# Kernel tuning notes

Measured on AMD Instinct MI355X. Metric: run time of the kernel, lower is better.

## Reference

```python
import jax, jax.numpy as jnp
import numpy as np

N_NODES = 50000
N_EDGES = 800000
D = 128
BN_EPS = 1e-5


def setup_inputs() -> dict:
    key = jax.random.key(0)
    ks = jax.random.split(key, 8)
    scale = 1.0 / np.sqrt(D)
    return {
        "nfeat": jax.random.normal(ks[0], (N_NODES, D), dtype=jnp.float32),
        "efeat": jax.random.normal(ks[1], (N_EDGES, D), dtype=jnp.float32),
        "src": jax.random.randint(ks[2], (N_EDGES,), 0, N_NODES, dtype=jnp.int32),
        "dst": jax.random.randint(ks[3], (N_EDGES,), 0, N_NODES, dtype=jnp.int32),
        "W1": jax.random.normal(ks[4], (D, D), dtype=jnp.float32) * scale,
        "b1": jnp.zeros((D,), dtype=jnp.float32),
        "gamma": jnp.ones((D,), dtype=jnp.float32),
        "beta": jnp.zeros((D,), dtype=jnp.float32),
        "W2": jax.random.normal(ks[5], (D, D), dtype=jnp.float32) * scale,
        "b2": jnp.zeros((D,), dtype=jnp.float32),
        "We": jax.random.normal(ks[6], (D, D), dtype=jnp.float32) * scale,
        "be": jnp.zeros((D,), dtype=jnp.float32),
    }


def reference(nfeat, efeat, src, dst, W1, b1, gamma, beta, W2, b2, We, be):
    n = nfeat.shape[0]
    # GINConv, sum aggregator, eps=0: h = (1+eps)*x + sum_{j in N(i)} x_j
    agg = jax.ops.segment_sum(nfeat[src], dst, num_segments=n)  # [N, D]
    h = nfeat + agg
    # apply_func: Linear -> BatchNorm1d (training-mode batch stats) -> ReLU -> Linear
    h = h @ W1 + b1
    mu = jnp.mean(h, axis=0)
    var = jnp.mean(jnp.square(h - mu), axis=0)  # biased variance, as BatchNorm uses
    h = gamma * (h - mu) * jax.lax.rsqrt(var + BN_EPS) + beta
    h = jax.nn.relu(h)
    h = h @ W2 + b2
    # edge branch: linear on edge feats, scatter-sum to destination nodes, residual add
    e = efeat @ We + be                                          # [E, D]
    h_e = jax.ops.segment_sum(e, dst, num_segments=n)            # [N, D]
    return h + h_e
```

## Files before the change

### kernel.cpp

```cpp
#include <hip/hip_runtime.h>

#define D 128

typedef __attribute__((ext_vector_type(8))) short bf16x8;
typedef __attribute__((ext_vector_type(4))) float f32x4;
typedef __attribute__((ext_vector_type(4))) float fx4;
typedef __attribute__((ext_vector_type(4))) short sx4;

static __device__ __forceinline__ short f2bf(float f) {
    union { float f; unsigned u; } v; v.f = f;
    const unsigned r = v.u + 0x7FFFu + ((v.u >> 16) & 1u);
    return (short)(r >> 16);
}
static __device__ __forceinline__ float bf2f(short s) {
    union { unsigned u; float f; } v;
    v.u = ((unsigned)(unsigned short)s) << 16;
    return v.f;
}

__global__ __launch_bounds__(256) void k_prep(
    const float* __restrict__ nfeat, short* __restrict__ nfb,
    const float* __restrict__ W1, const float* __restrict__ W2,
    const float* __restrict__ We, short* __restrict__ Wt1,
    short* __restrict__ Wt2, short* __restrict__ Wte,
    int* __restrict__ cnt, float* __restrict__ stats,
    int N, int nbConv, int nbW)
{
    const int b = blockIdx.x, t = threadIdx.x;
    if (b < nbConv) {
        const int i = b * 256 + t;
        if (i < (N * D) / 4) {
            const float4 v = ((const float4*)nfeat)[i];
            short4 s;
            s.x = f2bf(v.x); s.y = f2bf(v.y); s.z = f2bf(v.z); s.w = f2bf(v.w);
            ((short4*)nfb)[i] = s;
        }
    } else if (b < nbConv + nbW) {
        const int i = (b - nbConv) * 256 + t;
        const int m = i >> 14;
        const int idx = i & 16383;
        const int k = idx >> 7, n = idx & 127;
        const float* W = (m == 0) ? W1 : (m == 1) ? W2 : We;
        short* Wt = (m == 0) ? Wt1 : (m == 1) ? Wt2 : Wte;
        Wt[n * 128 + k] = f2bf(W[k * 128 + n]);
    } else {
        const int i = (b - nbConv - nbW) * 256 + t;
        if (i * 4 < N) ((int4*)cnt)[i] = make_int4(0, 0, 0, 0);
        if (b == nbConv + nbW && t < 256) stats[t] = 0.f;
    }
}

__global__ void k_hist(const int* __restrict__ dst, int* __restrict__ cnt, int E) {
    const int base = (blockIdx.x * 256 + threadIdx.x) * 4;
    if (base + 3 < E) {
        const int4 d4 = *(const int4*)(dst + base);
        atomicAdd(&cnt[d4.x], 1);
        atomicAdd(&cnt[d4.y], 1);
        atomicAdd(&cnt[d4.z], 1);
        atomicAdd(&cnt[d4.w], 1);
    } else {
        for (int e = base; e < E; ++e) atomicAdd(&cnt[dst[e]], 1);
    }
}

__global__ __launch_bounds__(1024) void k_scan(
    const int* __restrict__ cnt, int* __restrict__ row_ptr,
    int* __restrict__ cursor, float* __restrict__ degf, int N)
{
    __shared__ int ws[17];
    const int t = threadIdx.x, lane = t & 63, wid = t >> 6;
    int carry = 0;
    const int ntiles = (N + 4095) / 4096;
    for (int tile = 0; tile < ntiles; ++tile) {
        const int base = tile * 4096 + t * 4;
        int4 v = make_int4(0, 0, 0, 0);
        if (base + 3 < N) v = *(const int4*)(cnt + base);
        else {
            if (base     < N) v.x = cnt[base];
            if (base + 1 < N) v.y = cnt[base + 1];
            if (base + 2 < N) v.z = cnt[base + 2];
            if (base + 3 < N) v.w = cnt[base + 3];
        }
        const int s = v.x + v.y + v.z + v.w;
        int incl = s;
        #pragma unroll
        for (int off = 1; off < 64; off <<= 1) {
            const int u = __shfl_up(incl, off);
            if (lane >= off) incl += u;
        }
        if (lane == 63) ws[wid] = incl;
        __syncthreads();
        if (t < 16) {
            const int wv = ws[t];
            int wincl = wv;
            #pragma unroll
            for (int off = 1; off < 16; off <<= 1) {
                const int u = __shfl_up(wincl, off);
                if (t >= off) wincl += u;
            }
            ws[t] = wincl - wv;
            if (t == 15) ws[16] = wincl;
        }
        __syncthreads();
        const int ex = carry + ws[wid] + (incl - s);
        if (base + 3 < N) {
            const int4 rp = make_int4(ex, ex + v.x, ex + v.x + v.y,
                                      ex + v.x + v.y + v.z);
            *(int4*)(row_ptr + base) = rp;
            *(int4*)(cursor + base)  = rp;
            *(float4*)(degf + base)  =
                make_float4((float)v.x, (float)v.y, (float)v.z, (float)v.w);
        } else {
            int run = ex;
            if (base < N)     { row_ptr[base]   = run; cursor[base]   = run; degf[base]   = (float)v.x; run += v.x; }
            if (base + 1 < N) { row_ptr[base+1] = run; cursor[base+1] = run; degf[base+1] = (float)v.y; run += v.y; }
            if (base + 2 < N) { row_ptr[base+2] = run; cursor[base+2] = run; degf[base+2] = (float)v.z; run += v.z; }
            if (base + 3 < N) { row_ptr[base+3] = run; cursor[base+3] = run; degf[base+3] = (float)v.w; }
        }
        carry += ws[16];
        __syncthreads();
    }
    if (t == 0) row_ptr[N] = carry;
}

__global__ void k_scatter(const int* __restrict__ src, const int* __restrict__ dst,
                          int* __restrict__ cursor,
                          int2* __restrict__ epair, int E) {
    const int base = (blockIdx.x * 256 + threadIdx.x) * 4;
    if (base + 3 < E) {
        const int4 d4 = *(const int4*)(dst + base);
        const int4 s4 = *(const int4*)(src + base);
        int p;
        p = atomicAdd(&cursor[d4.x], 1); epair[p] = make_int2(base + 0, s4.x);
        p = atomicAdd(&cursor[d4.y], 1); epair[p] = make_int2(base + 1, s4.y);
        p = atomicAdd(&cursor[d4.z], 1); epair[p] = make_int2(base + 2, s4.z);
        p = atomicAdd(&cursor[d4.w], 1); epair[p] = make_int2(base + 3, s4.w);
    } else {
        for (int e = base; e < E; ++e) {
            const int p = atomicAdd(&cursor[dst[e]], 1);
            epair[p] = make_int2(e, src[e]);
        }
    }
}

__global__ __launch_bounds__(256) void k_gather(
    const short* __restrict__ nfb, const float* __restrict__ efeat,
    const int* __restrict__ row_ptr, const int2* __restrict__ epair,
    short* __restrict__ xbuf, short* __restrict__ agg_e, int N)
{
    const int t = threadIdx.x;
    const int c = t & 31;
    const int node = blockIdx.x * 8 + (t >> 5);
    if (node >= N) return;

    const int start = row_ptr[node];
    const int end   = row_ptr[node + 1];

    fx4 an = {0.f, 0.f, 0.f, 0.f};
    fx4 ae = {0.f, 0.f, 0.f, 0.f};
    int e = start;
    for (; e + 3 < end; e += 4) {
        const int2 p0 = epair[e];
        const int2 p1 = epair[e + 1];
        const int2 p2 = epair[e + 2];
        const int2 p3 = epair[e + 3];
        const fx4 ev0 = __builtin_nontemporal_load((const fx4*)(efeat + (size_t)p0.x * D) + c);
        const fx4 ev1 = __builtin_nontemporal_load((const fx4*)(efeat + (size_t)p1.x * D) + c);
        const fx4 ev2 = __builtin_nontemporal_load((const fx4*)(efeat + (size_t)p2.x * D) + c);
        const fx4 ev3 = __builtin_nontemporal_load((const fx4*)(efeat + (size_t)p3.x * D) + c);
        const sx4 nv0 = *((const sx4*)(nfb + (size_t)p0.y * D) + c);
        const sx4 nv1 = *((const sx4*)(nfb + (size_t)p1.y * D) + c);
        const sx4 nv2 = *((const sx4*)(nfb + (size_t)p2.y * D) + c);
        const sx4 nv3 = *((const sx4*)(nfb + (size_t)p3.y * D) + c);
        #pragma unroll
        for (int j = 0; j < 4; ++j) {
            ae[j] += (ev0[j] + ev1[j]) + (ev2[j] + ev3[j]);
            an[j] += (bf2f(nv0[j]) + bf2f(nv1[j])) + (bf2f(nv2[j]) + bf2f(nv3[j]));
        }
    }
    for (; e < end; ++e) {
        const int2 p0 = epair[e];
        const fx4 ev0 = __builtin_nontemporal_load((const fx4*)(efeat + (size_t)p0.x * D) + c);
        const sx4 nv0 = *((const sx4*)(nfb + (size_t)p0.y * D) + c);
        #pragma unroll
        for (int j = 0; j < 4; ++j) {
            ae[j] += ev0[j];
            an[j] += bf2f(nv0[j]);
        }
    }

    const sx4 self = *((const sx4*)(nfb + (size_t)node * D) + c);
    sx4 xv, ev2;
    #pragma unroll
    for (int j = 0; j < 4; ++j) {
        xv[j]  = f2bf(bf2f(self[j]) + an[j]);
        ev2[j] = f2bf(ae[j]);
    }
    __builtin_nontemporal_store(xv,  (sx4*)(xbuf  + (size_t)node * D) + c);
    __builtin_nontemporal_store(ev2, (sx4*)(agg_e + (size_t)node * D) + c);
}

__global__ __launch_bounds__(256) void k_h1(const short* xbuf,
                                            const short* __restrict__ Wt1,
                                            const float* __restrict__ b1,
                                            short* h1,
                                            float* __restrict__ stats, int N) {
    const int t = threadIdx.x;
    const int lane = t & 63;
    const int w = t >> 6;
    const int l15 = lane & 15;
    const int kg = lane >> 4;
    const int row0 = blockIdx.x * 64;

    bf16x8 bfr[4][2];
    #pragma unroll
    for (int kt = 0; kt < 4; ++kt)
        #pragma unroll
        for (int cf = 0; cf < 2; ++cf)
            bfr[kt][cf] = *(const bf16x8*)(Wt1 + (w * 32 + cf * 16 + l15) * D +
                                           kt * 32 + kg * 8);

    f32x4 acc[4][2];
    #pragma unroll
    for (int rt = 0; rt < 4; ++rt) { acc[rt][0] = (f32x4)0.f; acc[rt][1] = (f32x4)0.f; }

    #pragma unroll
    for (int rt = 0; rt < 4; ++rt) {
        const int row = row0 + rt * 16 + l15;
        bf16x8 a0 = (bf16x8)(short)0, a1 = a0, a2 = a0, a3 = a0;
        if (row < N) {
            const short* xp = xbuf + (size_t)row * D + kg * 8;
            a0 = *(const bf16x8*)(xp);
            a1 = *(const bf16x8*)(xp + 32);
            a2 = *(const bf16x8*)(xp + 64);
            a3 = *(const bf16x8*)(xp + 96);
        }
        acc[rt][0] = __builtin_amdgcn_mfma_f32_16x16x32_bf16(a0, bfr[0][0], acc[rt][0], 0, 0, 0);
        acc[rt][1] = __builtin_amdgcn_mfma_f32_16x16x32_bf16(a0, bfr[0][1], acc[rt][1], 0, 0, 0);
        acc[rt][0] = __builtin_amdgcn_mfma_f32_16x16x32_bf16(a1, bfr[1][0], acc[rt][0], 0, 0, 0);
        acc[rt][1] = __builtin_amdgcn_mfma_f32_16x16x32_bf16(a1, bfr[1][1], acc[rt][1], 0, 0, 0);
        acc[rt][0] = __builtin_amdgcn_mfma_f32_16x16x32_bf16(a2, bfr[2][0], acc[rt][0], 0, 0, 0);
        acc[rt][1] = __builtin_amdgcn_mfma_f32_16x16x32_bf16(a2, bfr[2][1], acc[rt][1], 0, 0, 0);
        acc[rt][0] = __builtin_amdgcn_mfma_f32_16x16x32_bf16(a3, bfr[3][0], acc[rt][0], 0, 0, 0);
        acc[rt][1] = __builtin_amdgcn_mfma_f32_16x16x32_bf16(a3, bfr[3][1], acc[rt][1], 0, 0, 0);
    }

    const float bias0 = b1[w * 32 + l15];
    const float bias1 = b1[w * 32 + 16 + l15];
    float cs0 = 0.f, cq0 = 0.f, cs1 = 0.f, cq1 = 0.f;
    #pragma unroll
    for (int rt = 0; rt < 4; ++rt) {
        #pragma unroll
        for (int j = 0; j < 4; ++j) {
            const int row = row0 + rt * 16 + kg * 4 + j;
            if (row < N) {
                const float h0 = acc[rt][0][j] + bias0;
                const float hv = acc[rt][1][j] + bias1;
                h1[(size_t)row * D + w * 32 + l15]      = f2bf(h0);
                h1[(size_t)row * D + w * 32 + 16 + l15] = f2bf(hv);
                cs0 += h0; cq0 += h0 * h0;
                cs1 += hv; cq1 += hv * hv;
            }
        }
    }
    #pragma unroll
    for (int m = 16; m < 64; m <<= 1) {
        cs0 += __shfl_xor(cs0, m); cq0 += __shfl_xor(cq0, m);
        cs1 += __shfl_xor(cs1, m); cq1 += __shfl_xor(cq1, m);
    }
    if (lane < 16) {
        atomicAdd(stats + w * 32 + lane,            cs0);
        atomicAdd(stats + w * 32 + 16 + lane,       cs1);
        atomicAdd(stats + 128 + w * 32 + lane,      cq0);
        atomicAdd(stats + 128 + w * 32 + 16 + lane, cq1);
    }
}

__global__ __launch_bounds__(256) void k_out(const short* __restrict__ h1,
                                             const short* __restrict__ agg_e,
                                             const short* __restrict__ Wt2,
                                             const short* __restrict__ Wte,
                                             const float* __restrict__ stats,
                                             const float* __restrict__ gamma,
                                             const float* __restrict__ beta,
                                             const float* __restrict__ b2,
                                             const float* __restrict__ be,
                                             const float* __restrict__ degf,
                                             float* __restrict__ out, int N) {
    __shared__ float scs[128], shs[128];
    const int t = threadIdx.x;
    if (t < 128) {
        const float invN = 1.0f / (float)N;
        const float mu = stats[t] * invN;
        const float var = stats[128 + t] * invN - mu * mu;
        const float sc = gamma[t] * rsqrtf(var + 1e-5f);
        scs[t] = sc;
        shs[t] = beta[t] - mu * sc;
    }
    __syncthreads();

    const int lane = t & 63;
    const int w = t >> 6;
    const int l15 = lane & 15;
    const int kg = lane >> 4;
    const int row0 = blockIdx.x * 64;

    f32x4 acc[4][2];
    #pragma unroll
    for (int rt = 0; rt < 4; ++rt) { acc[rt][0] = (f32x4)0.f; acc[rt][1] = (f32x4)0.f; }

    bf16x8 bfr[4][2];

    #pragma unroll
    for (int kt = 0; kt < 4; ++kt)
        #pragma unroll
        for (int cf = 0; cf < 2; ++cf)
            bfr[kt][cf] = *(const bf16x8*)(Wt2 + (w * 32 + cf * 16 + l15) * D +
                                           kt * 32 + kg * 8);

    #pragma unroll
    for (int rt = 0; rt < 4; ++rt) {
        const int row = row0 + rt * 16 + l15;
        #pragma unroll
        for (int kt = 0; kt < 4; ++kt) {
            bf16x8 raw = (bf16x8)(short)0;
            if (row < N)
                raw = *(const bf16x8*)(h1 + (size_t)row * D + kt * 32 + kg * 8);
            const int k0 = kt * 32 + kg * 8;
            const float4 sa = *(const float4*)(scs + k0);
            const float4 sb = *(const float4*)(scs + k0 + 4);
            const float4 ha = *(const float4*)(shs + k0);
            const float4 hb = *(const float4*)(shs + k0 + 4);
            bf16x8 afr;
            afr[0] = f2bf(fmaxf(bf2f(raw[0]) * sa.x + ha.x, 0.f));
            afr[1] = f2bf(fmaxf(bf2f(raw[1]) * sa.y + ha.y, 0.f));
            afr[2] = f2bf(fmaxf(bf2f(raw[2]) * sa.z + ha.z, 0.f));
            afr[3] = f2bf(fmaxf(bf2f(raw[3]) * sa.w + ha.w, 0.f));
            afr[4] = f2bf(fmaxf(bf2f(raw[4]) * sb.x + hb.x, 0.f));
            afr[5] = f2bf(fmaxf(bf2f(raw[5]) * sb.y + hb.y, 0.f));
            afr[6] = f2bf(fmaxf(bf2f(raw[6]) * sb.z + hb.z, 0.f));
            afr[7] = f2bf(fmaxf(bf2f(raw[7]) * sb.w + hb.w, 0.f));
            acc[rt][0] = __builtin_amdgcn_mfma_f32_16x16x32_bf16(afr, bfr[kt][0], acc[rt][0], 0, 0, 0);
            acc[rt][1] = __builtin_amdgcn_mfma_f32_16x16x32_bf16(afr, bfr[kt][1], acc[rt][1], 0, 0, 0);
        }
    }

    #pragma unroll
    for (int kt = 0; kt < 4; ++kt)
        #pragma unroll
        for (int cf = 0; cf < 2; ++cf)
            bfr[kt][cf] = *(const bf16x8*)(Wte + (w * 32 + cf * 16 + l15) * D +
                                           kt * 32 + kg * 8);

    #pragma unroll
    for (int rt = 0; rt < 4; ++rt) {
        const int row = row0 + rt * 16 + l15;
        bf16x8 a0 = (bf16x8)(short)0, a1 = a0, a2 = a0, a3 = a0;
        if (row < N) {
            const short* ap = agg_e + (size_t)row * D + kg * 8;
            a0 = *(const bf16x8*)(ap);
            a1 = *(const bf16x8*)(ap + 32);
            a2 = *(const bf16x8*)(ap + 64);
            a3 = *(const bf16x8*)(ap + 96);
        }
        acc[rt][0] = __builtin_amdgcn_mfma_f32_16x16x32_bf16(a0, bfr[0][0], acc[rt][0], 0, 0, 0);
        acc[rt][1] = __builtin_amdgcn_mfma_f32_16x16x32_bf16(a0, bfr[0][1], acc[rt][1], 0, 0, 0);
        acc[rt][0] = __builtin_amdgcn_mfma_f32_16x16x32_bf16(a1, bfr[1][0], acc[rt][0], 0, 0, 0);
        acc[rt][1] = __builtin_amdgcn_mfma_f32_16x16x32_bf16(a1, bfr[1][1], acc[rt][1], 0, 0, 0);
        acc[rt][0] = __builtin_amdgcn_mfma_f32_16x16x32_bf16(a2, bfr[2][0], acc[rt][0], 0, 0, 0);
        acc[rt][1] = __builtin_amdgcn_mfma_f32_16x16x32_bf16(a2, bfr[2][1], acc[rt][1], 0, 0, 0);
        acc[rt][0] = __builtin_amdgcn_mfma_f32_16x16x32_bf16(a3, bfr[3][0], acc[rt][0], 0, 0, 0);
        acc[rt][1] = __builtin_amdgcn_mfma_f32_16x16x32_bf16(a3, bfr[3][1], acc[rt][1], 0, 0, 0);
    }

    const float b2_0 = b2[w * 32 + l15];
    const float b2_1 = b2[w * 32 + 16 + l15];
    const float be_0 = be[w * 32 + l15];
    const float be_1 = be[w * 32 + 16 + l15];
    #pragma unroll
    for (int rt = 0; rt < 4; ++rt) {
        const int rbase = row0 + rt * 16 + kg * 4;
        float dgv[4];
        if (rbase + 3 < N) {
            *(float4*)dgv = *(const float4*)(degf + rbase);
        } else {
            #pragma unroll
            for (int j = 0; j < 4; ++j)
                dgv[j] = (rbase + j < N) ? degf[rbase + j] : 0.f;
        }
        #pragma unroll
        for (int j = 0; j < 4; ++j) {
            const int row = rbase + j;
            if (row < N) {
                out[(size_t)row * D + w * 32 + l15] =
                    acc[rt][0][j] + b2_0 + dgv[j] * be_0;
                out[(size_t)row * D + w * 32 + 16 + l15] =
                    acc[rt][1][j] + b2_1 + dgv[j] * be_1;
            }
        }
    }
}

extern "C" void kernel_launch(void* const* d_in, const int* in_sizes, int n_in,
                              void* d_out, int out_size, void* d_ws, size_t ws_size,
                              hipStream_t stream) {
    const float* nfeat = (const float*)d_in[0];
    const float* efeat = (const float*)d_in[1];
    const int*   src   = (const int*)d_in[2];
    const int*   dst   = (const int*)d_in[3];
    const float* W1    = (const float*)d_in[4];
    const float* b1    = (const float*)d_in[5];
    const float* gamma = (const float*)d_in[6];
    const float* beta  = (const float*)d_in[7];
    const float* W2    = (const float*)d_in[8];
    const float* b2    = (const float*)d_in[9];
    const float* We    = (const float*)d_in[10];
    const float* be    = (const float*)d_in[11];
    float* out = (float*)d_out;

    const int N = in_sizes[0] / D;
    const int E = in_sizes[2];
    const size_t ND = (size_t)N * D;

    short* nfb    = (short*)d_ws;
    short* xbuf   = nfb + ND;
    short* h1     = xbuf;
    short* agg_e  = xbuf + ND;
    short* Wt1    = agg_e + ND;
    short* Wt2    = Wt1 + 16384;
    short* Wte    = Wt2 + 16384;
    float* stats  = (float*)(Wte + 16384);
    float* degf   = stats + 256;
    int*   row_ptr= (int*)(degf + N);
    int*   cursor = row_ptr + (N + 16);
    int*   cnt    = cursor + (N + 16);
    int2*  epair  = (int2*)(cnt + (N + 16));

    const int nbConv = ((N * D) / 4 + 255) / 256;
    const int nbW    = 192;
    const int nbZ    = (N / 4 + 255) / 256;
    const int ebl4   = (E / 4 + 255) / 256;
    const int nb     = (N + 63) / 64;

    k_prep<<<nbConv + nbW + nbZ, 256, 0, stream>>>(nfeat, nfb, W1, W2, We,
                                                   Wt1, Wt2, Wte, cnt, stats,
                                                   N, nbConv, nbW);
    k_hist<<<ebl4, 256, 0, stream>>>(dst, cnt, E);
    k_scan<<<1, 1024, 0, stream>>>(cnt, row_ptr, cursor, degf, N);
    k_scatter<<<ebl4, 256, 0, stream>>>(src, dst, cursor, epair, E);
    k_gather<<<(N + 7) / 8, 256, 0, stream>>>(nfb, efeat, row_ptr, epair,
                                              xbuf, agg_e, N);
    k_h1<<<nb, 256, 0, stream>>>(xbuf, Wt1, b1, h1, stats, N);
    k_out<<<nb, 256, 0, stream>>>(h1, agg_e, Wt2, Wte, stats, gamma, beta,
                                  b2, be, degf, out, N);
}
```

Baseline: 285.5 us.

## Permute edge features into CSR order as bf16 before per-node summation

The scatter kernel now records each edge's CSR position and source index separately. A new k_perm kernel streams efeat sequentially, converts it to bf16 and writes it to a dst-sorted buffer. The summation kernel then reads contiguous edge rows, two edges per 32-lane group, and combines the halves with shuffles. This replaces random fp32 gathers of efeat with a coalesced read plus a scattered half-size write and a contiguous re-read. It adds an extra kernel, an extra bf16 buffer pass and bf16 rounding of each edge feature before summation.

```diff
diff --git a/kernel.cpp b/kernel.cpp
--- a/kernel.cpp
+++ b/kernel.cpp
@@ -6,6 +6,7 @@
 typedef __attribute__((ext_vector_type(4))) float f32x4;
 typedef __attribute__((ext_vector_type(4))) float fx4;
 typedef __attribute__((ext_vector_type(4))) short sx4;
+typedef __attribute__((ext_vector_type(8))) short sx8;
 
 static __device__ __forceinline__ short f2bf(float f) {
     union { float f; unsigned u; } v; v.f = f;
@@ -125,79 +126,100 @@
 
 __global__ void k_scatter(const int* __restrict__ src, const int* __restrict__ dst,
                           int* __restrict__ cursor,
-                          int2* __restrict__ epair, int E) {
+                          int* __restrict__ pos, int* __restrict__ esrcc, int E) {
     const int base = (blockIdx.x * 256 + threadIdx.x) * 4;
     if (base + 3 < E) {
         const int4 d4 = *(const int4*)(dst + base);
         const int4 s4 = *(const int4*)(src + base);
-        int p;
-        p = atomicAdd(&cursor[d4.x], 1); epair[p] = make_int2(base + 0, s4.x);
-        p = atomicAdd(&cursor[d4.y], 1); epair[p] = make_int2(base + 1, s4.y);
-        p = atomicAdd(&cursor[d4.z], 1); epair[p] = make_int2(base + 2, s4.z);
-        p = atomicAdd(&cursor[d4.w], 1); epair[p] = make_int2(base + 3, s4.w);
+        int4 p4;
+        p4.x = atomicAdd(&cursor[d4.x], 1); esrcc[p4.x] = s4.x;
+        p4.y = atomicAdd(&cursor[d4.y], 1); esrcc[p4.y] = s4.y;
+        p4.z = atomicAdd(&cursor[d4.z], 1); esrcc[p4.z] = s4.z;
+        p4.w = atomicAdd(&cursor[d4.w], 1); esrcc[p4.w] = s4.w;
+        *(int4*)(pos + base) = p4;
     } else {
         for (int e = base; e < E; ++e) {
             const int p = atomicAdd(&cursor[dst[e]], 1);
-            epair[p] = make_int2(e, src[e]);
-        }
-    }
-}
-
-__global__ __launch_bounds__(256) void k_gather(
-    const short* __restrict__ nfb, const float* __restrict__ efeat,
-    const int* __restrict__ row_ptr, const int2* __restrict__ epair,
+            esrcc[p] = src[e];
+            pos[e] = p;
+        }
+    }
+}
+
+__global__ __launch_bounds__(256) void k_perm(
+    const float* __restrict__ efeat, const int* __restrict__ pos,
+    short* __restrict__ ecsr, int E)
+{
+    const int t = threadIdx.x;
+    const int e = blockIdx.x * 16 + (t >> 4);
+    const int l = t & 15;
+    if (e >= E) return;
+    const float* ep = efeat + (size_t)e * D + l * 8;
+    const fx4 v0 = __builtin_nontemporal_load((const fx4*)ep);
+    const fx4 v1 = __builtin_nontemporal_load((const fx4*)ep + 1);
+    sx8 o;
+    o[0] = f2bf(v0[0]); o[1] = f2bf(v0[1]); o[2] = f2bf(v0[2]); o[3] = f2bf(v0[3]);
+    o[4] = f2bf(v1[0]); o[5] = f2bf(v1[1]); o[6] = f2bf(v1[2]); o[7] = f2bf(v1[3]);
+    const int p = pos[e];
+    *(sx8*)(ecsr + (size_t)p * D + l * 8) = o;
+}
+
+__global__ __launch_bounds__(256) void k_sum(
+    const short* __restrict__ nfb, const short* __restrict__ ecsr,
+    const int* __restrict__ row_ptr, const int* __restrict__ esrcc,
     short* __restrict__ xbuf, short* __restrict__ agg_e, int N)
 {
     const int t = threadIdx.x;
-    const int c = t & 31;
+    const int L = t & 31;
+    const int hl = L & 15;
+    const int rs = L >> 4;
     const int node = blockIdx.x * 8 + (t >> 5);
     if (node >= N) return;
 
     const int start = row_ptr[node];
     const int end   = row_ptr[node + 1];
 
-    fx4 an = {0.f, 0.f, 0.f, 0.f};
-    fx4 ae = {0.f, 0.f, 0.f, 0.f};
+    float an[8], ae[8];
+    #pragma unroll
+    for (int j = 0; j < 8; ++j) { an[j] = 0.f; ae[j] = 0.f; }
+
     int e = start;
-    for (; e + 3 < end; e += 4) {
-        const int2 p0 = epair[e];
-        const int2 p1 = epair[e + 1];
-        const int2 p2 = epair[e + 2];
-        const int2 p3 = epair[e + 3];
-        const fx4 ev0 = __builtin_nontemporal_load((const fx4*)(efeat + (size_t)p0.x * D) + c);
-        const fx4 ev1 = __builtin_nontemporal_load((const fx4*)(efeat + (size_t)p1.x * D) + c);
-        const fx4 ev2 = __builtin_nontemporal_load((const fx4*)(efeat + (size_t)p2.x * D) + c);
-        const fx4 ev3 = __builtin_nontemporal_load((const fx4*)(efeat + (size_t)p3.x * D) + c);
-        const sx4 nv0 = *((const sx4*)(nfb + (size_t)p0.y * D) + c);
-        const sx4 nv1 = *((const sx4*)(nfb + (size_t)p1.y * D) + c);
-        const sx4 nv2 = *((const sx4*)(nfb + (size_t)p2.y * D) + c);
-        const sx4 nv3 = *((const sx4*)(nfb + (size_t)p3.y * D) + c);
-        #pragma unroll
-        for (int j = 0; j < 4; ++j) {
-            ae[j] += (ev0[j] + ev1[j]) + (ev2[j] + ev3[j]);
-            an[j] += (bf2f(nv0[j]) + bf2f(nv1[j])) + (bf2f(nv2[j]) + bf2f(nv3[j]));
-        }
-    }
-    for (; e < end; ++e) {
-        const int2 p0 = epair[e];
-        const fx4 ev0 = __builtin_nontemporal_load((const fx4*)(efeat + (size_t)p0.x * D) + c);
-        const sx4 nv0 = *((const sx4*)(nfb + (size_t)p0.y * D) + c);
-        #pragma unroll
-        for (int j = 0; j < 4; ++j) {
-            ae[j] += ev0[j];
-            an[j] += bf2f(nv0[j]);
-        }
-    }
-
-    const sx4 self = *((const sx4*)(nfb + (size_t)node * D) + c);
-    sx4 xv, ev2;
-    #pragma unroll
-    for (int j = 0; j < 4; ++j) {
-        xv[j]  = f2bf(bf2f(self[j]) + an[j]);
-        ev2[j] = f2bf(ae[j]);
-    }
-    __builtin_nontemporal_store(xv,  (sx4*)(xbuf  + (size_t)node * D) + c);
-    __builtin_nontemporal_store(ev2, (sx4*)(agg_e + (size_t)node * D) + c);
+    for (; e + 1 < end; e += 2) {
+        const sx8 ev = *(const sx8*)(ecsr + (size_t)e * D + L * 8);
+        const int s = esrcc[e + rs];
+        const sx8 nv = *(const sx8*)(nfb + (size_t)s * D + hl * 8);
+        #pragma unroll
+        for (int j = 0; j < 8; ++j) {
+            ae[j] += bf2f(ev[j]);
+            an[j] += bf2f(nv[j]);
+        }
+    }
+    if (e < end && rs == 0) {
+        const sx8 ev = *(const sx8*)(ecsr + (size_t)e * D + hl * 8);
+        const int s = esrcc[e];
+        const sx8 nv = *(const sx8*)(nfb + (size_t)s * D + hl * 8);
+        #pragma unroll
+        for (int j = 0; j < 8; ++j) {
+            ae[j] += bf2f(ev[j]);
+            an[j] += bf2f(nv[j]);
+        }
+    }
+    #pragma unroll
+    for (int j = 0; j < 8; ++j) {
+        an[j] += __shfl_xor(an[j], 16);
+        ae[j] += __shfl_xor(ae[j], 16);
+    }
+    if (rs == 0) {
+        const sx8 self = *(const sx8*)(nfb + (size_t)node * D + hl * 8);
+        sx8 xv, ev2;
+        #pragma unroll
+        for (int j = 0; j < 8; ++j) {
+            xv[j]  = f2bf(bf2f(self[j]) + an[j]);
+            ev2[j] = f2bf(ae[j]);
+        }
+        *(sx8*)(xbuf  + (size_t)node * D + hl * 8) = xv;
+        *(sx8*)(agg_e + (size_t)node * D + hl * 8) = ev2;
+    }
 }
 
 __global__ __launch_bounds__(256) void k_h1(const short* xbuf,
@@ -434,7 +456,9 @@
     int*   row_ptr= (int*)(degf + N);
     int*   cursor = row_ptr + (N + 16);
     int*   cnt    = cursor + (N + 16);
-    int2*  epair  = (int2*)(cnt + (N + 16));
+    int*   pos    = cnt + (N + 16);
+    int*   esrcc  = pos + E;
+    short* ecsr   = (short*)(esrcc + E);
 
     const int nbConv = ((N * D) / 4 + 255) / 256;
     const int nbW    = 192;
@@ -447,9 +471,10 @@
                                                    N, nbConv, nbW);
     k_hist<<<ebl4, 256, 0, stream>>>(dst, cnt, E);
     k_scan<<<1, 1024, 0, stream>>>(cnt, row_ptr, cursor, degf, N);
-    k_scatter<<<ebl4, 256, 0, stream>>>(src, dst, cursor, epair, E);
-    k_gather<<<(N + 7) / 8, 256, 0, stream>>>(nfb, efeat, row_ptr, epair,
-                                              xbuf, agg_e, N);
+    k_scatter<<<ebl4, 256, 0, stream>>>(src, dst, cursor, pos, esrcc, E);
+    k_perm<<<(E + 15) / 16, 256, 0, stream>>>(efeat, pos, ecsr, E);
+    k_sum<<<(N + 7) / 8, 256, 0, stream>>>(nfb, ecsr, row_ptr, esrcc,
+                                           xbuf, agg_e, N);
     k_h1<<<nb, 256, 0, stream>>>(xbuf, Wt1, b1, h1, stats, N);
     k_out<<<nb, 256, 0, stream>>>(h1, agg_e, Wt2, Wte, stats, gamma, beta,
                                   b2, be, degf, out, N);
```

Result: slower. 352.7 us (+23.5%).
